# Optimization experiments

Hardware: AMD Instinct MI355X
Metric: run time of the kernel (lower is better)

The kernel has to match this reference:

```python
import jax, jax.numpy as jnp
import numpy as np

NUM_CLASSES = 1000
MARGIN = 1.0
COS_EPS = 1e-8   # torch F.cosine_similarity eps
NORM_EPS = 1e-12 # torch F.normalize eps


def setup_inputs() -> dict:
    key = jax.random.key(0)
    k1, k2 = jax.random.split(key)
    N, D = 65536, 256
    embeddings = jax.random.normal(k1, (N, D), dtype=jnp.float32)
    labels = jax.random.randint(k2, (N,), 0, NUM_CLASSES)
    return {"embeddings": embeddings, "labels": labels}


def reference(embeddings, labels):
    N = embeddings.shape[0]
    # L2-normalize embeddings (torch F.normalize with eps clamp on norm)
    e_norm = jnp.maximum(jnp.linalg.norm(embeddings, axis=1, keepdims=True), NORM_EPS)
    e = embeddings / e_norm  # [N, D], unit rows

    # Per-class mean of normalized embeddings; zero vector for empty classes
    sums = jax.ops.segment_sum(e, labels, num_segments=NUM_CLASSES)          # [C, D]
    counts = jax.ops.segment_sum(jnp.ones((N,), e.dtype), labels,
                                 num_segments=NUM_CLASSES)                    # [C]
    centers = sums / jnp.maximum(counts, 1.0)[:, None]                        # [C, D]

    # cosine_similarity(e_i, center_j) = (e_i . c_j) / max(||e_i||*||c_j||, eps)
    # ||e_i|| == 1 (up to the normalize clamp), so denom = max(||c_j||, eps)
    c_norm = jnp.linalg.norm(centers, axis=1)                                 # [C]
    denom = jnp.maximum(c_norm, COS_EPS)
    sims = (e @ centers.T) / denom[None, :]                                   # [N, C]

    rows = jnp.arange(N)
    pos = jnp.square(sims[rows, labels] - 1.0)                                # [N]
    neg_all = jnp.square(jax.nn.relu(MARGIN - sims))                          # [N, C]
    neg_at_label = neg_all[rows, labels]                                      # [N]
    neg = (neg_all.sum(axis=1) - neg_at_label) / (NUM_CLASSES - 1)            # [N]

    return jnp.mean(pos + neg)
```

## Files before the change

### kernel.cpp

```cpp
#include <hip/hip_runtime.h>
#include <hip/hip_bf16.h>

#define NROWS 65536
#define DIM   256
#define NCLS  1000
#define CPAD  1024

typedef __attribute__((ext_vector_type(8))) short bf16x8;
typedef __attribute__((ext_vector_type(4))) float f32x4;

__device__ inline unsigned short f2bf(float x) {
    unsigned int u = __builtin_bit_cast(unsigned int, x);
    unsigned int lsb = (u >> 16) & 1u;
    u += 0x7fffu + lsb;
    return (unsigned short)(u >> 16);
}

__device__ inline float bf2f(unsigned short u) {
    unsigned int v = ((unsigned int)u) << 16;
    return __builtin_bit_cast(float, v);
}

__device__ inline void gload_lds16(const void* g, void* l) {
    __builtin_amdgcn_global_load_lds(
        (const __attribute__((address_space(1))) unsigned int*)g,
        (__attribute__((address_space(3))) unsigned int*)l, 16, 0, 0);
}

__global__ __launch_bounds__(256) void k_norm_acc(
    const float* __restrict__ emb, unsigned short* __restrict__ e,
    float* __restrict__ sums, unsigned int* __restrict__ counts,
    float* __restrict__ acc, unsigned int* __restrict__ done)
{
    const int tid = threadIdx.x;
    const int bid = blockIdx.x;
    if (tid < 128) sums[bid * 128 + tid] = 0.0f;
    if (bid < 16 && tid < 64) counts[bid * 64 + tid] = 0u;
    if (bid == 0 && tid == 0) { *acc = 0.0f; *done = 0u; }

    const int wave = tid >> 6, lane = tid & 63;
    const int w = bid * 4 + wave;

    #pragma unroll
    for (int i = 0; i < 2; ++i) {
        const int rbase = w * 8 + i * 4;
        float4 v[4];
        #pragma unroll
        for (int r = 0; r < 4; ++r)
            v[r] = ((const float4*)(emb + (size_t)(rbase + r) * DIM))[lane];
        float ss[4];
        #pragma unroll
        for (int r = 0; r < 4; ++r)
            ss[r] = v[r].x*v[r].x + v[r].y*v[r].y + v[r].z*v[r].z + v[r].w*v[r].w;
        #pragma unroll
        for (int off = 1; off < 64; off <<= 1) {
            #pragma unroll
            for (int r = 0; r < 4; ++r) ss[r] += __shfl_xor(ss[r], off);
        }
        #pragma unroll
        for (int r = 0; r < 4; ++r) {
            float inv = 1.0f / fmaxf(sqrtf(ss[r]), 1e-12f);
            ushort4 u;
            u.x = f2bf(v[r].x * inv); u.y = f2bf(v[r].y * inv);
            u.z = f2bf(v[r].z * inv); u.w = f2bf(v[r].w * inv);
            ((ushort4*)(e + (size_t)(rbase + r) * DIM))[lane] = u;
        }
    }
}

__global__ __launch_bounds__(256) void k_gather_partial(
    const unsigned short* __restrict__ e, const int* __restrict__ labels,
    float* __restrict__ sums, unsigned int* __restrict__ counts)
{
    const int c   = blockIdx.x >> 1;
    const int h   = blockIdx.x & 1;
    const int tid = threadIdx.x;
    const int wave = tid >> 6, lane = tid & 63;

    __shared__ float part[4][DIM];
    __shared__ unsigned int cnt_s[4];

    const int base = h * (NROWS / 2);
    float a0 = 0.f, a1 = 0.f, a2 = 0.f, a3 = 0.f;
    unsigned int cnt = 0;

    for (int it = 0; it < (NROWS / 2) / 256 / 8; ++it) {
        int lb[8];
        #pragma unroll
        for (int u = 0; u < 8; ++u)
            lb[u] = labels[base + (it * 8 + u) * 256 + wave * 64 + lane];
        #pragma unroll
        for (int u = 0; u < 8; ++u) {
            unsigned long long m = __ballot(lb[u] == c);
            cnt += (unsigned int)__popcll(m);
            int rb = base + (it * 8 + u) * 256 + wave * 64;
            while (m) {
                int b = __ffsll((long long)m) - 1;  m &= m - 1;
                ushort4 v = ((const ushort4*)(e + (size_t)(rb + b) * DIM))[lane];
                a0 += bf2f(v.x); a1 += bf2f(v.y); a2 += bf2f(v.z); a3 += bf2f(v.w);
            }
        }
    }
    ((float4*)part[wave])[lane] = make_float4(a0, a1, a2, a3);
    if (lane == 0) cnt_s[wave] = cnt;
    __syncthreads();

    float s = part[0][tid] + part[1][tid] + part[2][tid] + part[3][tid];
    atomicAdd(&sums[(size_t)c * DIM + tid], s);
    if (tid == 0)
        atomicAdd(&counts[c], cnt_s[0] + cnt_s[1] + cnt_s[2] + cnt_s[3]);
}

__global__ __launch_bounds__(256) void k_centers(
    const float* __restrict__ sums, const unsigned int* __restrict__ counts,
    unsigned short* __restrict__ cs)
{
    int gid  = blockIdx.x * 256 + threadIdx.x;
    int c    = gid >> 6;
    int lane = gid & 63;
    float4 v = ((const float4*)(sums + (size_t)c * DIM))[lane];
    float ic = 1.0f / fmaxf((float)counts[c], 1.0f);
    v.x *= ic; v.y *= ic; v.z *= ic; v.w *= ic;
    float ss = v.x*v.x + v.y*v.y + v.z*v.z + v.w*v.w;
    #pragma unroll
    for (int off = 1; off < 64; off <<= 1) ss += __shfl_xor(ss, off);
    float sc = 1.0f / fmaxf(sqrtf(ss), 1e-8f);
    ushort4 u;
    u.x = f2bf(v.x * sc); u.y = f2bf(v.y * sc);
    u.z = f2bf(v.z * sc); u.w = f2bf(v.w * sc);
    ((ushort4*)(cs + (size_t)c * DIM))[lane] = u;
}

#define TMB 128
#define TCB 128

__global__ __launch_bounds__(256, 2) void k_loss_mfma(
    const unsigned short* __restrict__ e, const unsigned short* __restrict__ cs,
    const int* __restrict__ labels, float* __restrict__ acc,
    unsigned int* __restrict__ done, float* __restrict__ out)
{
    __shared__ __align__(16) unsigned short b_s[4][TCB * 64];
    __shared__ float red_s[4];

    const int tid  = threadIdx.x;
    const int row0 = blockIdx.x * TMB;
    const int wave = tid >> 6, lane = tid & 63;
    const int l16 = lane & 15, q = lane >> 4;
    const int st_r = lane >> 3;
    const int st_s = (lane & 7) ^ st_r;

    int labv[8];
    #pragma unroll
    for (int mi = 0; mi < 2; ++mi)
        #pragma unroll
        for (int rg = 0; rg < 4; ++rg)
            labv[mi * 4 + rg] = labels[row0 + wave*32 + mi*16 + q*4 + rg];

    bf16x8 af[4][2][2];
    #pragma unroll
    for (int mi = 0; mi < 2; ++mi) {
        const unsigned short* pa =
            e + (size_t)(row0 + wave*32 + mi*16 + l16) * DIM + q * 8;
        #pragma unroll
        for (int kc = 0; kc < 4; ++kc)
            #pragma unroll
            for (int kk = 0; kk < 2; ++kk)
                af[kc][mi][kk] = *(const bf16x8*)(pa + kc*64 + kk*32);
    }

    #pragma unroll
    for (int pt = 0; pt < 3; ++pt)
        #pragma unroll
        for (int ch = 0; ch < 4; ++ch) {
            int chunk = wave * 4 + ch;
            gload_lds16(&cs[(size_t)(chunk*8 + st_r) * DIM + pt*64 + st_s*8],
                        &b_s[pt][chunk * 512]);
        }
    __syncthreads();

    float la_bulk = 0.0f, la_corr = 0.0f;
    const float KN = 1.0f / 999.0f;

    for (int cb = 0; cb < CPAD / TCB; ++cb) {
        f32x4 accf[2][8];
        #pragma unroll
        for (int mi = 0; mi < 2; ++mi)
            #pragma unroll
            for (int ni = 0; ni < 8; ++ni)
                accf[mi][ni] = (f32x4){0.f, 0.f, 0.f, 0.f};

        #pragma unroll
        for (int kc = 0; kc < 4; ++kc) {
            __builtin_amdgcn_sched_barrier(0);
            asm volatile("s_waitcnt vmcnt(8)" ::: "memory");
            __builtin_amdgcn_s_barrier();
            __builtin_amdgcn_sched_barrier(0);

            {
                const int t2  = cb * 4 + kc + 3;
                const int cb2 = t2 >> 2, kc2 = t2 & 3;
                #pragma unroll
                for (int ch = 0; ch < 4; ++ch) {
                    int chunk = wave * 4 + ch;
                    int crow  = (cb2 * TCB + chunk * 8 + st_r) & (CPAD - 1);
                    gload_lds16(&cs[(size_t)crow * DIM + kc2*64 + st_s*8],
                                &b_s[kc2][chunk * 512]);
                }
            }

            #pragma unroll
            for (int kk = 0; kk < 2; ++kk) {
                bf16x8 bfr[8];
                #pragma unroll
                for (int ni = 0; ni < 8; ++ni) {
                    int rowB = ni * 16 + l16;
                    bfr[ni] = *(const bf16x8*)&b_s[kc][
                        rowB * 64 + (((kk*4 + q) ^ (rowB & 7)) * 8)];
                }
                #pragma unroll
                for (int mi = 0; mi < 2; ++mi)
                    #pragma unroll
                    for (int ni = 0; ni < 8; ++ni)
                        accf[mi][ni] = __builtin_amdgcn_mfma_f32_16x16x32_bf16(
                            af[kc][mi][kk], bfr[ni], accf[mi][ni], 0, 0, 0);
            }
        }

        #pragma unroll
        for (int mi = 0; mi < 2; ++mi)
            #pragma unroll
            for (int rg = 0; rg < 4; ++rg) {
                #pragma unroll
                for (int ni = 0; ni < 8; ++ni) {
                    float t = 1.0f - accf[mi][ni][rg];
                    la_bulk += t * t;
                }
                int lr = labv[mi*4 + rg] - cb*TCB - l16;
                if ((lr & ~112) == 0) {
                    int nih = lr >> 4;
                    float sv = (nih & 4)
                        ? ((nih & 2) ? ((nih & 1) ? accf[mi][7][rg] : accf[mi][6][rg])
                                     : ((nih & 1) ? accf[mi][5][rg] : accf[mi][4][rg]))
                        : ((nih & 2) ? ((nih & 1) ? accf[mi][3][rg] : accf[mi][2][rg])
                                     : ((nih & 1) ? accf[mi][1][rg] : accf[mi][0][rg]));
                    float t = 1.0f - sv;
                    la_corr += t * t;
                }
            }
    }

    float la = la_bulk * KN + la_corr * (1.0f - KN);
    #pragma unroll
    for (int off = 32; off >= 1; off >>= 1) la += __shfl_xor(la, off);
    if (lane == 0) red_s[wave] = la;
    __syncthreads();
    if (tid == 0) {
        atomicAdd(acc, red_s[0] + red_s[1] + red_s[2] + red_s[3]);
        __threadfence();
        unsigned int t = atomicAdd(done, 1u);
        if (t == (unsigned int)(NROWS / TMB) - 1u) {
            float v = atomicAdd(acc, 0.0f);
            out[0] = v * (1.0f / (float)NROWS) - 24.0f * (1.0f / 999.0f);
        }
    }
}

extern "C" void kernel_launch(void* const* d_in, const int* in_sizes, int n_in,
                              void* d_out, int out_size, void* d_ws, size_t ws_size,
                              hipStream_t stream)
{
    const float* emb    = (const float*)d_in[0];
    const int*   labels = (const int*)d_in[1];
    float*       out    = (float*)d_out;
    char*        ws     = (char*)d_ws;

    const size_t OFF_CS   = (size_t)NROWS * DIM * 2;
    const size_t OFF_SUMS = OFF_CS + (size_t)CPAD * DIM * 2;
    const size_t OFF_CNT  = OFF_SUMS + (size_t)CPAD * DIM * 4;
    const size_t OFF_ACC  = OFF_CNT + (size_t)CPAD * 4;
    const size_t OFF_DONE = OFF_ACC + 16;

    unsigned short* e      = (unsigned short*)ws;
    unsigned short* cs     = (unsigned short*)(ws + OFF_CS);
    float*          sums   = (float*)(ws + OFF_SUMS);
    unsigned int*   counts = (unsigned int*)(ws + OFF_CNT);
    float*          acc    = (float*)(ws + OFF_ACC);
    unsigned int*   done   = (unsigned int*)(ws + OFF_DONE);

    k_norm_acc      <<<NROWS / 32, 256, 0, stream>>>(emb, e, sums, counts, acc, done);
    k_gather_partial<<<NCLS * 2, 256, 0, stream>>>(e, labels, sums, counts);
    k_centers       <<<CPAD / 4, 256, 0, stream>>>(sums, counts, cs);
    k_loss_mfma     <<<NROWS / TMB, 256, 0, stream>>>(e, cs, labels, acc, done, out);
}
```

Baseline: 160.7 us.

## Stage embedding tile in LDS and stream center fragments from global per wave

The loss kernel is restructured to use 256-row by 256-class tiles with 512 threads arranged as a 2x4 wave grid. The embedding tile is now loaded once into swizzled LDS. Center fragments are read directly from global memory (L2-resident) into registers, replacing the old triple-buffered LDS pipeline for centers. This removes the per-k-step barriers and the async center prefetch, and gives each wave an 8x4 MFMA tile. In exchange, center loads are issued without software pipelining, which risks exposed global-load latency, and register pressure rises from the larger accumulator set.

```diff
diff --git a/kernel.cpp b/kernel.cpp
--- a/kernel.cpp
+++ b/kernel.cpp
@@ -131,118 +131,95 @@
     ((ushort4*)(cs + (size_t)c * DIM))[lane] = u;
 }
 
-#define TMB 128
-#define TCB 128
-
-__global__ __launch_bounds__(256, 2) void k_loss_mfma(
+#define TMB 256
+#define TCB 256
+
+__global__ __launch_bounds__(512, 2) void k_loss_mfma(
     const unsigned short* __restrict__ e, const unsigned short* __restrict__ cs,
     const int* __restrict__ labels, float* __restrict__ acc,
     unsigned int* __restrict__ done, float* __restrict__ out)
 {
-    __shared__ __align__(16) unsigned short b_s[4][TCB * 64];
-    __shared__ float red_s[4];
+    __shared__ __align__(16) unsigned short a_s[4][TMB * 64];
+    __shared__ float red_s[8];
 
     const int tid  = threadIdx.x;
     const int row0 = blockIdx.x * TMB;
     const int wave = tid >> 6, lane = tid & 63;
+    const int wm = wave >> 2, wn = wave & 3;
     const int l16 = lane & 15, q = lane >> 4;
     const int st_r = lane >> 3;
     const int st_s = (lane & 7) ^ st_r;
 
-    int labv[8];
-    #pragma unroll
-    for (int mi = 0; mi < 2; ++mi)
+    #pragma unroll
+    for (int kc = 0; kc < 4; ++kc)
+        #pragma unroll
+        for (int ch = 0; ch < 4; ++ch) {
+            int c2 = wave * 4 + ch;
+            gload_lds16(&e[(size_t)(row0 + c2*8 + st_r) * DIM + kc*64 + st_s*8],
+                        &a_s[kc][c2 * 512]);
+        }
+
+    int labv[32];
+    #pragma unroll
+    for (int mi = 0; mi < 8; ++mi)
         #pragma unroll
         for (int rg = 0; rg < 4; ++rg)
-            labv[mi * 4 + rg] = labels[row0 + wave*32 + mi*16 + q*4 + rg];
-
-    bf16x8 af[4][2][2];
-    #pragma unroll
-    for (int mi = 0; mi < 2; ++mi) {
-        const unsigned short* pa =
-            e + (size_t)(row0 + wave*32 + mi*16 + l16) * DIM + q * 8;
-        #pragma unroll
-        for (int kc = 0; kc < 4; ++kc)
-            #pragma unroll
-            for (int kk = 0; kk < 2; ++kk)
-                af[kc][mi][kk] = *(const bf16x8*)(pa + kc*64 + kk*32);
-    }
-
-    #pragma unroll
-    for (int pt = 0; pt < 3; ++pt)
-        #pragma unroll
-        for (int ch = 0; ch < 4; ++ch) {
-            int chunk = wave * 4 + ch;
-            gload_lds16(&cs[(size_t)(chunk*8 + st_r) * DIM + pt*64 + st_s*8],
-                        &b_s[pt][chunk * 512]);
-        }
+            labv[mi*4 + rg] = labels[row0 + wm*128 + mi*16 + q*4 + rg];
+
     __syncthreads();
 
     float la_bulk = 0.0f, la_corr = 0.0f;
     const float KN = 1.0f / 999.0f;
 
     for (int cb = 0; cb < CPAD / TCB; ++cb) {
-        f32x4 accf[2][8];
-        #pragma unroll
-        for (int mi = 0; mi < 2; ++mi)
-            #pragma unroll
-            for (int ni = 0; ni < 8; ++ni)
+        f32x4 accf[8][4];
+        #pragma unroll
+        for (int mi = 0; mi < 8; ++mi)
+            #pragma unroll
+            for (int ni = 0; ni < 4; ++ni)
                 accf[mi][ni] = (f32x4){0.f, 0.f, 0.f, 0.f};
 
+        const unsigned short* bbase =
+            cs + (size_t)(cb*TCB + wn*64 + l16) * DIM + q * 8;
+
         #pragma unroll
         for (int kc = 0; kc < 4; ++kc) {
-            __builtin_amdgcn_sched_barrier(0);
-            asm volatile("s_waitcnt vmcnt(8)" ::: "memory");
-            __builtin_amdgcn_s_barrier();
-            __builtin_amdgcn_sched_barrier(0);
-
-            {
-                const int t2  = cb * 4 + kc + 3;
-                const int cb2 = t2 >> 2, kc2 = t2 & 3;
-                #pragma unroll
-                for (int ch = 0; ch < 4; ++ch) {
-                    int chunk = wave * 4 + ch;
-                    int crow  = (cb2 * TCB + chunk * 8 + st_r) & (CPAD - 1);
-                    gload_lds16(&cs[(size_t)crow * DIM + kc2*64 + st_s*8],
-                                &b_s[kc2][chunk * 512]);
+            #pragma unroll
+            for (int kk = 0; kk < 2; ++kk) {
+                bf16x8 bfr[4];
+                #pragma unroll
+                for (int ni = 0; ni < 4; ++ni)
+                    bfr[ni] = *(const bf16x8*)(bbase + ni*16*DIM + kc*64 + kk*32);
+                bf16x8 afv[8];
+                #pragma unroll
+                for (int mi = 0; mi < 8; ++mi) {
+                    int rowA = wm*128 + mi*16 + l16;
+                    afv[mi] = *(const bf16x8*)&a_s[kc][
+                        rowA*64 + (((kk*4 + q) ^ (rowA & 7)) * 8)];
                 }
+                #pragma unroll
+                for (int mi = 0; mi < 8; ++mi)
+                    #pragma unroll
+                    for (int ni = 0; ni < 4; ++ni)
+                        accf[mi][ni] = __builtin_amdgcn_mfma_f32_16x16x32_bf16(
+                            afv[mi], bfr[ni], accf[mi][ni], 0, 0, 0);
             }
-
-            #pragma unroll
-            for (int kk = 0; kk < 2; ++kk) {
-                bf16x8 bfr[8];
-                #pragma unroll
-                for (int ni = 0; ni < 8; ++ni) {
-                    int rowB = ni * 16 + l16;
-                    bfr[ni] = *(const bf16x8*)&b_s[kc][
-                        rowB * 64 + (((kk*4 + q) ^ (rowB & 7)) * 8)];
-                }
-                #pragma unroll
-                for (int mi = 0; mi < 2; ++mi)
-                    #pragma unroll
-                    for (int ni = 0; ni < 8; ++ni)
-                        accf[mi][ni] = __builtin_amdgcn_mfma_f32_16x16x32_bf16(
-                            af[kc][mi][kk], bfr[ni], accf[mi][ni], 0, 0, 0);
-            }
-        }
-
-        #pragma unroll
-        for (int mi = 0; mi < 2; ++mi)
+        }
+
+        #pragma unroll
+        for (int mi = 0; mi < 8; ++mi)
             #pragma unroll
             for (int rg = 0; rg < 4; ++rg) {
                 #pragma unroll
-                for (int ni = 0; ni < 8; ++ni) {
+                for (int ni = 0; ni < 4; ++ni) {
                     float t = 1.0f - accf[mi][ni][rg];
                     la_bulk += t * t;
                 }
-                int lr = labv[mi*4 + rg] - cb*TCB - l16;
-                if ((lr & ~112) == 0) {
+                int lr = labv[mi*4 + rg] - cb*TCB - wn*64 - l16;
+                if ((lr & ~48) == 0) {
                     int nih = lr >> 4;
-                    float sv = (nih & 4)
-                        ? ((nih & 2) ? ((nih & 1) ? accf[mi][7][rg] : accf[mi][6][rg])
-                                     : ((nih & 1) ? accf[mi][5][rg] : accf[mi][4][rg]))
-                        : ((nih & 2) ? ((nih & 1) ? accf[mi][3][rg] : accf[mi][2][rg])
-                                     : ((nih & 1) ? accf[mi][1][rg] : accf[mi][0][rg]));
+                    float sv = (nih & 2) ? ((nih & 1) ? accf[mi][3][rg] : accf[mi][2][rg])
+                                         : ((nih & 1) ? accf[mi][1][rg] : accf[mi][0][rg]);
                     float t = 1.0f - sv;
                     la_corr += t * t;
                 }
@@ -255,7 +232,8 @@
     if (lane == 0) red_s[wave] = la;
     __syncthreads();
     if (tid == 0) {
-        atomicAdd(acc, red_s[0] + red_s[1] + red_s[2] + red_s[3]);
+        atomicAdd(acc, red_s[0] + red_s[1] + red_s[2] + red_s[3]
+                     + red_s[4] + red_s[5] + red_s[6] + red_s[7]);
         __threadfence();
         unsigned int t = atomicAdd(done, 1u);
         if (t == (unsigned int)(NROWS / TMB) - 1u) {
@@ -290,5 +268,5 @@
     k_norm_acc      <<<NROWS / 32, 256, 0, stream>>>(emb, e, sums, counts, acc, done);
     k_gather_partial<<<NCLS * 2, 256, 0, stream>>>(e, labels, sums, counts);
     k_centers       <<<CPAD / 4, 256, 0, stream>>>(sums, counts, cs);
-    k_loss_mfma     <<<NROWS / TMB, 256, 0, stream>>>(e, cs, labels, acc, done, out);
-}
+    k_loss_mfma     <<<NROWS / TMB, 512, 0, stream>>>(e, cs, labels, acc, done, out);
+}
```

New measurement: 320.2 us. +99.2%, slower.

## Batch four classes per gather block and shrink loss tile with 3-stage LDS ring

Applied to the files above, without the earlier changes.

The class-sum gather kernel now has each block handle four classes over one-eighth of the rows, instead of one class over half the rows. This cuts repeated label reads by reusing each label load across four ballots. The loss MFMA kernel halves its row tile to 64 and replaces the four-slot LDS buffer with a three-slot ring, prefetching two stages ahead. Together these lower LDS and register use so three blocks can fit per CU, at the cost of less reuse of each loaded center tile. Labels are packed two per register to save VGPRs.

```diff
diff --git a/kernel.cpp b/kernel.cpp
--- a/kernel.cpp
+++ b/kernel.cpp
@@ -72,43 +72,63 @@
     const unsigned short* __restrict__ e, const int* __restrict__ labels,
     float* __restrict__ sums, unsigned int* __restrict__ counts)
 {
-    const int c   = blockIdx.x >> 1;
-    const int h   = blockIdx.x & 1;
+    const int grp = blockIdx.x >> 3;
+    const int sl  = blockIdx.x & 7;
+    const int c0  = grp * 4;
     const int tid = threadIdx.x;
     const int wave = tid >> 6, lane = tid & 63;
 
-    __shared__ float part[4][DIM];
-    __shared__ unsigned int cnt_s[4];
-
-    const int base = h * (NROWS / 2);
-    float a0 = 0.f, a1 = 0.f, a2 = 0.f, a3 = 0.f;
-    unsigned int cnt = 0;
-
-    for (int it = 0; it < (NROWS / 2) / 256 / 8; ++it) {
+    __shared__ float part[4][4][DIM];
+    __shared__ unsigned int cnt_s[4][4];
+
+    const int base = sl * (NROWS / 8);
+    float a[4][4];
+    #pragma unroll
+    for (int cl = 0; cl < 4; ++cl)
+        #pragma unroll
+        for (int d = 0; d < 4; ++d) a[cl][d] = 0.0f;
+    unsigned int cnt[4] = {0u, 0u, 0u, 0u};
+
+    for (int it = 0; it < (NROWS / 8) / 256 / 8; ++it) {
         int lb[8];
         #pragma unroll
         for (int u = 0; u < 8; ++u)
             lb[u] = labels[base + (it * 8 + u) * 256 + wave * 64 + lane];
         #pragma unroll
         for (int u = 0; u < 8; ++u) {
-            unsigned long long m = __ballot(lb[u] == c);
-            cnt += (unsigned int)__popcll(m);
             int rb = base + (it * 8 + u) * 256 + wave * 64;
-            while (m) {
-                int b = __ffsll((long long)m) - 1;  m &= m - 1;
-                ushort4 v = ((const ushort4*)(e + (size_t)(rb + b) * DIM))[lane];
-                a0 += bf2f(v.x); a1 += bf2f(v.y); a2 += bf2f(v.z); a3 += bf2f(v.w);
-            }
-        }
-    }
-    ((float4*)part[wave])[lane] = make_float4(a0, a1, a2, a3);
-    if (lane == 0) cnt_s[wave] = cnt;
+            #pragma unroll
+            for (int cl = 0; cl < 4; ++cl) {
+                unsigned long long m = __ballot(lb[u] == c0 + cl);
+                cnt[cl] += (unsigned int)__popcll(m);
+                while (m) {
+                    int b = __ffsll((long long)m) - 1;  m &= m - 1;
+                    ushort4 v = ((const ushort4*)(e + (size_t)(rb + b) * DIM))[lane];
+                    a[cl][0] += bf2f(v.x); a[cl][1] += bf2f(v.y);
+                    a[cl][2] += bf2f(v.z); a[cl][3] += bf2f(v.w);
+                }
+            }
+        }
+    }
+    #pragma unroll
+    for (int cl = 0; cl < 4; ++cl)
+        ((float4*)part[wave][cl])[lane] =
+            make_float4(a[cl][0], a[cl][1], a[cl][2], a[cl][3]);
+    if (lane == 0) {
+        cnt_s[wave][0] = cnt[0]; cnt_s[wave][1] = cnt[1];
+        cnt_s[wave][2] = cnt[2]; cnt_s[wave][3] = cnt[3];
+    }
     __syncthreads();
 
-    float s = part[0][tid] + part[1][tid] + part[2][tid] + part[3][tid];
-    atomicAdd(&sums[(size_t)c * DIM + tid], s);
-    if (tid == 0)
-        atomicAdd(&counts[c], cnt_s[0] + cnt_s[1] + cnt_s[2] + cnt_s[3]);
+    #pragma unroll
+    for (int cl = 0; cl < 4; ++cl) {
+        float s = part[0][cl][tid] + part[1][cl][tid]
+                + part[2][cl][tid] + part[3][cl][tid];
+        atomicAdd(&sums[(size_t)(c0 + cl) * DIM + tid], s);
+    }
+    if (tid < 4)
+        atomicAdd(&counts[c0 + tid], cnt_s[0][tid] + cnt_s[1][tid]
+                                   + cnt_s[2][tid] + cnt_s[3][tid]);
 }
 
 __global__ __launch_bounds__(256) void k_centers(
@@ -131,15 +151,15 @@
     ((ushort4*)(cs + (size_t)c * DIM))[lane] = u;
 }
 
-#define TMB 128
+#define TMB 64
 #define TCB 128
 
-__global__ __launch_bounds__(256, 2) void k_loss_mfma(
+__global__ __launch_bounds__(256, 3) void k_loss_mfma(
     const unsigned short* __restrict__ e, const unsigned short* __restrict__ cs,
     const int* __restrict__ labels, float* __restrict__ acc,
     unsigned int* __restrict__ done, float* __restrict__ out)
 {
-    __shared__ __align__(16) unsigned short b_s[4][TCB * 64];
+    __shared__ __align__(16) unsigned short b_s[3][TCB * 64];
     __shared__ float red_s[4];
 
     const int tid  = threadIdx.x;
@@ -149,104 +169,103 @@
     const int st_r = lane >> 3;
     const int st_s = (lane & 7) ^ st_r;
 
-    int labv[8];
-    #pragma unroll
-    for (int mi = 0; mi < 2; ++mi)
-        #pragma unroll
-        for (int rg = 0; rg < 4; ++rg)
-            labv[mi * 4 + rg] = labels[row0 + wave*32 + mi*16 + q*4 + rg];
-
-    bf16x8 af[4][2][2];
-    #pragma unroll
-    for (int mi = 0; mi < 2; ++mi) {
-        const unsigned short* pa =
-            e + (size_t)(row0 + wave*32 + mi*16 + l16) * DIM + q * 8;
-        #pragma unroll
-        for (int kc = 0; kc < 4; ++kc)
-            #pragma unroll
-            for (int kk = 0; kk < 2; ++kk)
-                af[kc][mi][kk] = *(const bf16x8*)(pa + kc*64 + kk*32);
-    }
-
-    #pragma unroll
-    for (int pt = 0; pt < 3; ++pt)
+    #pragma unroll
+    for (int pt = 0; pt < 2; ++pt)
         #pragma unroll
         for (int ch = 0; ch < 4; ++ch) {
             int chunk = wave * 4 + ch;
             gload_lds16(&cs[(size_t)(chunk*8 + st_r) * DIM + pt*64 + st_s*8],
                         &b_s[pt][chunk * 512]);
         }
+
+    int labp[2];
+    #pragma unroll
+    for (int p = 0; p < 2; ++p) {
+        int rr = row0 + wave*16 + q*4 + p*2;
+        labp[p] = labels[rr] | (labels[rr + 1] << 16);
+    }
+
+    bf16x8 af[4][2];
+    {
+        const unsigned short* pa =
+            e + (size_t)(row0 + wave*16 + l16) * DIM + q * 8;
+        #pragma unroll
+        for (int kc = 0; kc < 4; ++kc)
+            #pragma unroll
+            for (int kk = 0; kk < 2; ++kk)
+                af[kc][kk] = *(const bf16x8*)(pa + kc*64 + kk*32);
+    }
+
     __syncthreads();
 
     float la_bulk = 0.0f, la_corr = 0.0f;
     const float KN = 1.0f / 999.0f;
 
+    int cur0 = 0;
     for (int cb = 0; cb < CPAD / TCB; ++cb) {
-        f32x4 accf[2][8];
-        #pragma unroll
-        for (int mi = 0; mi < 2; ++mi)
-            #pragma unroll
-            for (int ni = 0; ni < 8; ++ni)
-                accf[mi][ni] = (f32x4){0.f, 0.f, 0.f, 0.f};
+        f32x4 accf[8];
+        #pragma unroll
+        for (int ni = 0; ni < 8; ++ni) accf[ni] = (f32x4){0.f, 0.f, 0.f, 0.f};
 
         #pragma unroll
         for (int kc = 0; kc < 4; ++kc) {
+            int cu = cur0 + kc;     if (cu >= 3) cu -= 3; if (cu >= 3) cu -= 3;
+            int sg = cur0 + kc + 2; if (sg >= 3) sg -= 3; if (sg >= 3) sg -= 3;
+
             __builtin_amdgcn_sched_barrier(0);
-            asm volatile("s_waitcnt vmcnt(8)" ::: "memory");
+            asm volatile("s_waitcnt vmcnt(4)" ::: "memory");
             __builtin_amdgcn_s_barrier();
             __builtin_amdgcn_sched_barrier(0);
 
             {
-                const int t2  = cb * 4 + kc + 3;
+                const int t2  = cb * 4 + kc + 2;
                 const int cb2 = t2 >> 2, kc2 = t2 & 3;
                 #pragma unroll
                 for (int ch = 0; ch < 4; ++ch) {
                     int chunk = wave * 4 + ch;
                     int crow  = (cb2 * TCB + chunk * 8 + st_r) & (CPAD - 1);
                     gload_lds16(&cs[(size_t)crow * DIM + kc2*64 + st_s*8],
-                                &b_s[kc2][chunk * 512]);
+                                &b_s[sg][chunk * 512]);
                 }
             }
 
+            const unsigned short* bs = b_s[cu];
             #pragma unroll
             for (int kk = 0; kk < 2; ++kk) {
                 bf16x8 bfr[8];
                 #pragma unroll
                 for (int ni = 0; ni < 8; ++ni) {
                     int rowB = ni * 16 + l16;
-                    bfr[ni] = *(const bf16x8*)&b_s[kc][
-                        rowB * 64 + (((kk*4 + q) ^ (rowB & 7)) * 8)];
+                    bfr[ni] = *(const bf16x8*)&bs[rowB * 64 + (((kk*4 + q) ^ (rowB & 7)) * 8)];
                 }
                 #pragma unroll
-                for (int mi = 0; mi < 2; ++mi)
-                    #pragma unroll
-                    for (int ni = 0; ni < 8; ++ni)
-                        accf[mi][ni] = __builtin_amdgcn_mfma_f32_16x16x32_bf16(
-                            af[kc][mi][kk], bfr[ni], accf[mi][ni], 0, 0, 0);
-            }
-        }
-
-        #pragma unroll
-        for (int mi = 0; mi < 2; ++mi)
-            #pragma unroll
-            for (int rg = 0; rg < 4; ++rg) {
-                #pragma unroll
-                for (int ni = 0; ni < 8; ++ni) {
-                    float t = 1.0f - accf[mi][ni][rg];
-                    la_bulk += t * t;
-                }
-                int lr = labv[mi*4 + rg] - cb*TCB - l16;
-                if ((lr & ~112) == 0) {
-                    int nih = lr >> 4;
-                    float sv = (nih & 4)
-                        ? ((nih & 2) ? ((nih & 1) ? accf[mi][7][rg] : accf[mi][6][rg])
-                                     : ((nih & 1) ? accf[mi][5][rg] : accf[mi][4][rg]))
-                        : ((nih & 2) ? ((nih & 1) ? accf[mi][3][rg] : accf[mi][2][rg])
-                                     : ((nih & 1) ? accf[mi][1][rg] : accf[mi][0][rg]));
-                    float t = 1.0f - sv;
-                    la_corr += t * t;
-                }
-            }
+                for (int ni = 0; ni < 8; ++ni)
+                    accf[ni] = __builtin_amdgcn_mfma_f32_16x16x32_bf16(
+                        af[kc][kk], bfr[ni], accf[ni], 0, 0, 0);
+            }
+        }
+
+        #pragma unroll
+        for (int rg = 0; rg < 4; ++rg) {
+            #pragma unroll
+            for (int ni = 0; ni < 8; ++ni) {
+                float t = 1.0f - accf[ni][rg];
+                la_bulk += t * t;
+            }
+            int lv = (labp[rg >> 1] >> ((rg & 1) * 16)) & 0xffff;
+            int lr = lv - cb*TCB - l16;
+            if ((lr & ~112) == 0) {
+                int nih = lr >> 4;
+                float sv = (nih & 4)
+                    ? ((nih & 2) ? ((nih & 1) ? accf[7][rg] : accf[6][rg])
+                                 : ((nih & 1) ? accf[5][rg] : accf[4][rg]))
+                    : ((nih & 2) ? ((nih & 1) ? accf[3][rg] : accf[2][rg])
+                                 : ((nih & 1) ? accf[1][rg] : accf[0][rg]));
+                float t = 1.0f - sv;
+                la_corr += t * t;
+            }
+        }
+        cur0 = (cur0 + 1 == 3) ? 0 : cur0 + 1;
     }
 
     float la = la_bulk * KN + la_corr * (1.0f - KN);
```

Measured after the change: 199.2 us. 24.0% more time.
